# Kernel optimization log

Hardware: AMD Instinct MI355X
Metric: run time of the kernel (lower is better)

## Reference

```python
import jax, jax.numpy as jnp
import numpy as np
from jax import lax

H = 1024        # lstm_hidden_size
V = 512         # action_vocab_size
WV = 300        # word_vec_size
S = 64          # step_num
N = 512         # entity_num


def setup_inputs() -> dict:
    key = jax.random.key(0)
    ks = jax.random.split(key, 16)
    s = 0.02
    return {
        "video_vectors": jax.random.normal(ks[0], (1, S, H), jnp.float32),
        "entity_vectors": jax.random.normal(ks[1], (N, H), jnp.float32),
        # action_selector: Linear(H,H) -> ReLU -> Dropout(eval: identity) -> Linear(H,V) -> Sigmoid
        "A1w": jax.random.normal(ks[2], (H, H), jnp.float32) * s,
        "A1b": jnp.zeros((H,), jnp.float32),
        "A2w": jax.random.normal(ks[3], (V, H), jnp.float32) * s,
        "A2b": jnp.zeros((V,), jnp.float32),
        "action_emb": jax.random.normal(ks[4], (V, WV), jnp.float32) * s,
        "W1w": jax.random.normal(ks[5], (H, H), jnp.float32) * s,
        "W1b": jnp.zeros((H,), jnp.float32),
        "W2w": jax.random.normal(ks[6], (H, H + V), jnp.float32) * s,
        "W2b": jnp.zeros((H,), jnp.float32),
        "W3w": jax.random.normal(ks[7], (3, H), jnp.float32) * s,
        "W3b": jnp.zeros((3,), jnp.float32),
        "W4w": jax.random.normal(ks[8], (1, WV), jnp.float32) * s,
        "W4b": jnp.zeros((1,), jnp.float32),
    }


def _forward(video_vectors, entity_vectors, A1w, A1b, A2w, A2b, action_emb,
             W1w, W1b, W2w, W2b, W3w, W3b, W4w, W4b):
    vv = video_vectors[0]                       # [S, H]
    n = entity_vectors.shape[0]

    def step(carry, v_ac):
        ev, prev_ent_attn = carry               # ev: [N, H], prev: [N]
        # action selector (dropout is identity in eval)
        h = jax.nn.relu(v_ac @ A1w.T + A1b)
        ac_prob = jax.nn.sigmoid(h @ A2w.T + A2b)        # [V]
        bar_ft = (ac_prob / ac_prob.sum()) @ action_emb  # [WV]
        hat_ht = jax.nn.relu(v_ac @ W1w.T + W1b)         # [H]
        w2v = jnp.concatenate([hat_ht, ac_prob]) @ W2w.T + W2b  # [H]
        ent_prob = jax.nn.sigmoid(ev @ w2v)              # [N]
        choice = jax.nn.softmax(hat_ht @ W3w.T + W3b)    # [3]
        attn = choice[0] * ent_prob + choice[1] * prev_ent_attn  # (choice[2]*0)
        bar_et = (attn / attn.sum()) @ ev                # [H]
        scal = bar_ft @ W4w[0] + W4b[0]                  # scalar (W4(bar_ft))
        kt = jax.nn.relu(scal * bar_et)                  # [H]
        ev_new = attn[:, None] * kt[None, :] + (1.0 - attn)[:, None] * ev  # [N, H]
        return (ev_new, ent_prob), (ent_prob, ac_prob, bar_et, ev_new, bar_ft)

    init = (entity_vectors, jnp.zeros((n,), entity_vectors.dtype))
    _, (ent_probs, ac_probs, step_ent, step_all, step_act) = lax.scan(step, init, vv)
    return ent_probs, ac_probs, step_ent, step_all, step_act


def reference(video_vectors, entity_vectors, A1w, A1b, A2w, A2b, action_emb,
              W1w, W1b, W2w, W2b, W3w, W3b, W4w, W4b):
    return _forward(video_vectors, entity_vectors, A1w, A1b, A2w, A2b, action_emb,
                    W1w, W1b, W2w, W2b, W3w, W3b, W4w, W4b)
```

## Files before the change

### kernel.cpp

```cpp
#include <hip/hip_runtime.h>

#define H  1024
#define V  512
#define WV 300
#define S  64
#define N  512

#define WS_HALL   0
#define WS_CAT    (S*H)
#define WS_W2V    (WS_CAT + S*1536)
#define WS_CHOICE (WS_W2V + S*H)
#define WS_SCAL   (WS_CHOICE + 2*S)
#define WS_ACSUM  (WS_SCAL + S)
#define WS_KT     (WS_ACSUM + S)
#define WS_ATT    (WS_KT + S*H)
#define WS_ACCUM  (WS_ATT + S*N)
#define WS_ASUM   (WS_ACCUM + 3*H)
#define WS_CTR    (WS_ASUM + 4)

#define OUT_EP   0
#define OUT_AC   (S*N)
#define OUT_SE   (S*N + S*V)
#define OUT_ALL  (OUT_SE + S*H)
#define OUT_ACT  (OUT_ALL + (size_t)S*N*H)

__device__ __forceinline__ float wave_reduce(float v) {
#pragma unroll
  for (int m = 32; m > 0; m >>= 1) v += __shfl_xor(v, m, 64);
  return v;
}
__device__ __forceinline__ float dot4(float4 a, float4 b) {
  return a.x*b.x + a.y*b.y + a.z*b.z + a.w*b.w;
}

#define KC 64
__global__ __launch_bounds__(256) void gemmNT(
    const float* __restrict__ X, int ldx,
    const float* __restrict__ W, const float* __restrict__ bias,
    int K, int act,
    float* __restrict__ out1, int ld1,
    float* __restrict__ out2, int ld2) {
  __shared__ float Xs[64][KC + 4];
  __shared__ float Ws[64][KC + 4];
  const int tid = threadIdx.x;
  const int tm = tid >> 5, tn = tid & 31;
  const int jbase = blockIdx.x * 64;
  float acc[8][2];
#pragma unroll
  for (int i = 0; i < 8; ++i) acc[i][0] = acc[i][1] = 0.f;
  const int lr = tid >> 2;
  const int lc = (tid & 3) * 16;
  for (int k0 = 0; k0 < K; k0 += KC) {
    const float4* xp = (const float4*)(X + (size_t)lr * ldx + k0 + lc);
    const float4* wp = (const float4*)(W + (size_t)(jbase + lr) * K + k0 + lc);
    float4 xv0 = xp[0], xv1 = xp[1], xv2 = xp[2], xv3 = xp[3];
    float4 wv0 = wp[0], wv1 = wp[1], wv2 = wp[2], wv3 = wp[3];
    __syncthreads();
    *(float4*)&Xs[lr][lc +  0] = xv0; *(float4*)&Xs[lr][lc +  4] = xv1;
    *(float4*)&Xs[lr][lc +  8] = xv2; *(float4*)&Xs[lr][lc + 12] = xv3;
    *(float4*)&Ws[lr][lc +  0] = wv0; *(float4*)&Ws[lr][lc +  4] = wv1;
    *(float4*)&Ws[lr][lc +  8] = wv2; *(float4*)&Ws[lr][lc + 12] = wv3;
    __syncthreads();
#pragma unroll
    for (int kk = 0; kk < KC; kk += 4) {
      float4 w0 = *(const float4*)&Ws[tn][kk];
      float4 w1 = *(const float4*)&Ws[tn + 32][kk];
#pragma unroll
      for (int i = 0; i < 8; ++i) {
        float4 x = *(const float4*)&Xs[tm * 8 + i][kk];
        acc[i][0] += dot4(x, w0);
        acc[i][1] += dot4(x, w1);
      }
    }
  }
  const int j0 = jbase + tn, j1 = jbase + tn + 32;
  const float b0 = bias[j0], b1 = bias[j1];
#pragma unroll
  for (int i = 0; i < 8; ++i) {
    const int r = tm * 8 + i;
    float v0 = acc[i][0] + b0;
    float v1 = acc[i][1] + b1;
    if (act == 1) { v0 = fmaxf(v0, 0.f); v1 = fmaxf(v1, 0.f); }
    else if (act == 2) {
      v0 = 1.f / (1.f + __expf(-v0));
      v1 = 1.f / (1.f + __expf(-v1));
    }
    out1[(size_t)r * ld1 + j0] = v0;
    out1[(size_t)r * ld1 + j1] = v1;
    if (out2) {
      out2[(size_t)r * ld2 + j0] = v0;
      out2[(size_t)r * ld2 + j1] = v1;
    }
  }
}

__global__ void k_choice(const float* __restrict__ cat, const float* __restrict__ out_ac,
                         const float* __restrict__ W3w, const float* __restrict__ W3b,
                         float* __restrict__ ws) {
  int t = blockIdx.x, tid = threadIdx.x;
  const float* hat = cat + (size_t)t * 1536;
  float4 h4 = *(const float4*)(hat + tid * 4);
  float p[4];
#pragma unroll
  for (int r = 0; r < 3; ++r) {
    float4 w4 = *(const float4*)(W3w + (size_t)r * H + tid * 4);
    p[r] = dot4(h4, w4);
  }
  const float* ac = out_ac + (size_t)t * V;
  p[3] = ac[tid * 2] + ac[tid * 2 + 1];
  __shared__ float red[4][256];
#pragma unroll
  for (int q = 0; q < 4; ++q) red[q][tid] = p[q];
  __syncthreads();
  for (int sft = 128; sft > 0; sft >>= 1) {
    if (tid < sft) {
#pragma unroll
      for (int q = 0; q < 4; ++q) red[q][tid] += red[q][tid + sft];
    }
    __syncthreads();
  }
  if (tid == 0) {
    float l0 = red[0][0] + W3b[0], l1 = red[1][0] + W3b[1], l2 = red[2][0] + W3b[2];
    float m  = fmaxf(l0, fmaxf(l1, l2));
    float e0 = __expf(l0 - m), e1 = __expf(l1 - m), e2 = __expf(l2 - m);
    float inv = 1.f / (e0 + e1 + e2);
    ws[WS_CHOICE + t * 2]     = e0 * inv;
    ws[WS_CHOICE + t * 2 + 1] = e1 * inv;
    ws[WS_ACSUM + t]          = red[3][0];
  }
}

__global__ __launch_bounds__(256) void k_barft(
    const float* __restrict__ out_ac, const float* __restrict__ emb,
    const float* __restrict__ ws_ro, const float* __restrict__ W4w,
    const float* __restrict__ W4b, float* __restrict__ out_act,
    float* __restrict__ ws) {
  int t = blockIdx.x, tid = threadIdx.x;
  __shared__ float acS[V];
  const float* ac = out_ac + (size_t)t * V;
  acS[tid] = ac[tid];
  acS[tid + 256] = ac[tid + 256];
  __syncthreads();
  float s0 = 0.f, s1 = 0.f;
  const int w0 = tid, w1 = 256 + tid;
  for (int v = 0; v < V; ++v) {
    float a = acS[v];
    const float* er = emb + (size_t)v * WV;
    s0 += a * er[w0];
    if (tid < WV - 256) s1 += a * er[w1];
  }
  float inv = 1.f / ws_ro[WS_ACSUM + t];
  s0 *= inv; s1 *= inv;
  out_act[(size_t)t * WV + w0] = s0;
  if (tid < WV - 256) out_act[(size_t)t * WV + w1] = s1;
  float p = s0 * W4w[w0] + (tid < WV - 256 ? s1 * W4w[w1] : 0.f);
  __shared__ float red[256];
  red[tid] = p;
  __syncthreads();
  for (int s = 128; s > 0; s >>= 1) {
    if (tid < s) red[tid] += red[tid + s];
    __syncthreads();
  }
  if (tid == 0) ws[WS_SCAL + t] = red[0] + W4b[0];
}

__global__ __launch_bounds__(256) void k_seq(
    const float* __restrict__ ev0, const float* __restrict__ ws,
    float* __restrict__ accum, float* __restrict__ asum, unsigned* __restrict__ ctr,
    float* __restrict__ att, float* __restrict__ ktb,
    float* __restrict__ out_ep, float* __restrict__ out_se) {
  const int g = blockIdx.x, tid = threadIdx.x;
  const int lane = tid & 63, wv = tid >> 6;
  const int col = tid * 4;
  __shared__ float attnS[8], prevS[8], red[8][4];
  if (tid < 8) prevS[tid] = 0.f;
  float4 ev[8];
#pragma unroll
  for (int r = 0; r < 8; ++r)
    ev[r] = *(const float4*)(ev0 + (size_t)(g * 8 + r) * H + col);
  __syncthreads();
  unsigned target = 0;
  for (int t = 0; t < S; ++t) {
    const float4 w4 = *(const float4*)(ws + WS_W2V + (size_t)t * H + col);
    float dp[8];
#pragma unroll
    for (int r = 0; r < 8; ++r) dp[r] = dot4(ev[r], w4);
#pragma unroll
    for (int r = 0; r < 8; ++r) {
#pragma unroll
      for (int m = 32; m > 0; m >>= 1) dp[r] += __shfl_xor(dp[r], m, 64);
    }
    if (lane == 0) {
#pragma unroll
      for (int r = 0; r < 8; ++r) red[r][wv] = dp[r];
    }
    __syncthreads();
    if (tid < 8) {
      float d  = red[tid][0] + red[tid][1] + red[tid][2] + red[tid][3];
      float ep = 1.f / (1.f + __expf(-d));
      out_ep[(size_t)t * N + g * 8 + tid] = ep;
      float a = ws[WS_CHOICE + 2 * t] * ep + ws[WS_CHOICE + 2 * t + 1] * prevS[tid];
      prevS[tid] = ep;
      attnS[tid] = a;
      att[(size_t)t * N + g * 8 + tid] = a;
    }
    __syncthreads();
    float at[8];
#pragma unroll
    for (int r = 0; r < 8; ++r) at[r] = attnS[r];
    float4 pv = make_float4(0.f, 0.f, 0.f, 0.f);
#pragma unroll
    for (int r = 0; r < 8; ++r) {
      pv.x += at[r] * ev[r].x; pv.y += at[r] * ev[r].y;
      pv.z += at[r] * ev[r].z; pv.w += at[r] * ev[r].w;
    }
    float* acc = accum + (t % 3) * H;
    atomicAdd(acc + col + 0, pv.x);
    atomicAdd(acc + col + 1, pv.y);
    atomicAdd(acc + col + 2, pv.z);
    atomicAdd(acc + col + 3, pv.w);
    if (tid == 0) {
      float pa = 0.f;
#pragma unroll
      for (int r = 0; r < 8; ++r) pa += at[r];
      atomicAdd(asum + (t % 3), pa);
    }
    __syncthreads();
    target += (unsigned)gridDim.x;
    if (tid == 0) {
      __hip_atomic_fetch_add(ctr, 1u, __ATOMIC_RELEASE, __HIP_MEMORY_SCOPE_AGENT);
      while (__hip_atomic_load(ctr, __ATOMIC_ACQUIRE, __HIP_MEMORY_SCOPE_AGENT) < target)
        __builtin_amdgcn_s_sleep(2);
    }
    __syncthreads();
    float asv = __hip_atomic_load(asum + (t % 3), __ATOMIC_RELAXED, __HIP_MEMORY_SCOPE_AGENT);
    float4 pvs;
    pvs.x = __hip_atomic_load(acc + col + 0, __ATOMIC_RELAXED, __HIP_MEMORY_SCOPE_AGENT);
    pvs.y = __hip_atomic_load(acc + col + 1, __ATOMIC_RELAXED, __HIP_MEMORY_SCOPE_AGENT);
    pvs.z = __hip_atomic_load(acc + col + 2, __ATOMIC_RELAXED, __HIP_MEMORY_SCOPE_AGENT);
    pvs.w = __hip_atomic_load(acc + col + 3, __ATOMIC_RELAXED, __HIP_MEMORY_SCOPE_AGENT);
    float inv = 1.f / asv;
    float4 bar = make_float4(pvs.x * inv, pvs.y * inv, pvs.z * inv, pvs.w * inv);
    float sc = ws[WS_SCAL + t];
    float4 kt = make_float4(fmaxf(sc * bar.x, 0.f), fmaxf(sc * bar.y, 0.f),
                            fmaxf(sc * bar.z, 0.f), fmaxf(sc * bar.w, 0.f));
    if (g == 0) {
      *(float4*)(out_se + (size_t)t * H + col) = bar;
      *(float4*)(ktb + (size_t)t * H + col) = kt;
    }
    if (tid < 16)
      __hip_atomic_store(accum + ((t + 2) % 3) * H + g * 16 + tid, 0.f,
                         __ATOMIC_RELAXED, __HIP_MEMORY_SCOPE_AGENT);
    if (g == 0 && tid == 16)
      __hip_atomic_store(asum + ((t + 2) % 3), 0.f, __ATOMIC_RELAXED, __HIP_MEMORY_SCOPE_AGENT);
#pragma unroll
    for (int r = 0; r < 8; ++r) {
      float a = at[r];
      ev[r].x = a * kt.x + (1.f - a) * ev[r].x;
      ev[r].y = a * kt.y + (1.f - a) * ev[r].y;
      ev[r].z = a * kt.z + (1.f - a) * ev[r].z;
      ev[r].w = a * kt.w + (1.f - a) * ev[r].w;
    }
  }
}

__global__ __launch_bounds__(256) void k_recon(
    const float* __restrict__ ev0, const float* __restrict__ att,
    const float* __restrict__ ktb, float* __restrict__ out_all) {
  const int n = blockIdx.x, tid = threadIdx.x;
  const int col = tid * 4;
  __shared__ float aS[S];
  if (tid < S) aS[tid] = att[(size_t)tid * N + n];
  float4 v = *(const float4*)(ev0 + (size_t)n * H + col);
  __syncthreads();
  for (int t = 0; t < S; ++t) {
    float a = aS[t];
    float4 k4 = *(const float4*)(ktb + (size_t)t * H + col);
    v.x = a * k4.x + (1.f - a) * v.x;
    v.y = a * k4.y + (1.f - a) * v.y;
    v.z = a * k4.z + (1.f - a) * v.z;
    v.w = a * k4.w + (1.f - a) * v.w;
    *(float4*)(out_all + ((size_t)t * N + n) * H + col) = v;
  }
}

extern "C" void kernel_launch(void* const* d_in, const int* in_sizes, int n_in,
                              void* d_out, int out_size, void* d_ws, size_t ws_size,
                              hipStream_t stream) {
  const float* vv  = (const float*)d_in[0];
  const float* ev0 = (const float*)d_in[1];
  const float* A1w = (const float*)d_in[2];
  const float* A1b = (const float*)d_in[3];
  const float* A2w = (const float*)d_in[4];
  const float* A2b = (const float*)d_in[5];
  const float* emb = (const float*)d_in[6];
  const float* W1w = (const float*)d_in[7];
  const float* W1b = (const float*)d_in[8];
  const float* W2w = (const float*)d_in[9];
  const float* W2b = (const float*)d_in[10];
  const float* W3w = (const float*)d_in[11];
  const float* W3b = (const float*)d_in[12];
  const float* W4w = (const float*)d_in[13];
  const float* W4b = (const float*)d_in[14];

  float* ws  = (float*)d_ws;
  float* out = (float*)d_out;
  float* out_ep  = out + OUT_EP;
  float* out_ac  = out + OUT_AC;
  float* out_se  = out + OUT_SE;
  float* out_all = out + OUT_ALL;
  float* out_act = out + OUT_ACT;
  float* cat = ws + WS_CAT;

  hipMemsetAsync(ws + WS_ACCUM, 0, (size_t)(3 * H + 5) * sizeof(float), stream);

  gemmNT<<<16, 256, 0, stream>>>(vv, H, A1w, A1b, H, 1, ws + WS_HALL, H, (float*)nullptr, 0);
  gemmNT<<<16, 256, 0, stream>>>(vv, H, W1w, W1b, H, 1, cat, 1536, (float*)nullptr, 0);
  gemmNT<<<8, 256, 0, stream>>>(ws + WS_HALL, H, A2w, A2b, H, 2, out_ac, V, cat + H, 1536);
  k_choice<<<S, 256, 0, stream>>>(cat, out_ac, W3w, W3b, ws);
  gemmNT<<<16, 256, 0, stream>>>(cat, 1536, W2w, W2b, 1536, 0, ws + WS_W2V, H, (float*)nullptr, 0);
  k_barft<<<S, 256, 0, stream>>>(out_ac, emb, ws, W4w, W4b, out_act, ws);
  k_seq<<<64, 256, 0, stream>>>(ev0, ws, ws + WS_ACCUM, ws + WS_ASUM,
                                (unsigned*)(ws + WS_CTR),
                                ws + WS_ATT, ws + WS_KT, out_ep, out_se);
  k_recon<<<N, 256, 0, stream>>>(ev0, ws + WS_ATT, ws + WS_KT, out_all);
}
```

Measured before the change: 1.380 ms.

## Batch input GEMMs into one launch, prefetch K tiles, spin without sleep

Merges the two independent GEMMs on the video vectors (A1 and W1) into a single launch using a 2D grid, which removes one kernel launch and lets both run concurrently. It also adds register prefetch of the next K chunk in the GEMM so global loads overlap with the shared-memory compute. The grid barrier in the sequential kernel now busy-spins with relaxed loads and no s_sleep, then does one acquire load, which should shorten barrier wake-up latency across 64 steps at the cost of heavier polling traffic.

After: 1.267 ms. 1.09x faster.

```diff
diff --git a/kernel.cpp b/kernel.cpp
--- a/kernel.cpp
+++ b/kernel.cpp
@@ -24,25 +24,31 @@
 #define OUT_ALL  (OUT_SE + S*H)
 #define OUT_ACT  (OUT_ALL + (size_t)S*N*H)
 
-__device__ __forceinline__ float wave_reduce(float v) {
-#pragma unroll
-  for (int m = 32; m > 0; m >>= 1) v += __shfl_xor(v, m, 64);
-  return v;
-}
 __device__ __forceinline__ float dot4(float4 a, float4 b) {
   return a.x*b.x + a.y*b.y + a.z*b.z + a.w*b.w;
 }
 
+struct GArgs {
+  const float* X; const float* W0; const float* W1;
+  const float* B0; const float* B1;
+  float* o1_0; float* o1_1; float* o2_0; float* o2_1;
+  int ldx, K, act, ld1_0, ld1_1, ld2_0, ld2_1;
+};
+
 #define KC 64
-__global__ __launch_bounds__(256) void gemmNT(
-    const float* __restrict__ X, int ldx,
-    const float* __restrict__ W, const float* __restrict__ bias,
-    int K, int act,
-    float* __restrict__ out1, int ld1,
-    float* __restrict__ out2, int ld2) {
+__global__ __launch_bounds__(256) void gemmNT(GArgs a) {
   __shared__ float Xs[64][KC + 4];
   __shared__ float Ws[64][KC + 4];
   const int tid = threadIdx.x;
+  const int m = blockIdx.y;
+  const float* W    = m ? a.W1 : a.W0;
+  const float* bias = m ? a.B1 : a.B0;
+  float* out1 = m ? a.o1_1 : a.o1_0;
+  float* out2 = m ? a.o2_1 : a.o2_0;
+  const int ld1 = m ? a.ld1_1 : a.ld1_0;
+  const int ld2 = m ? a.ld2_1 : a.ld2_0;
+  const int K = a.K;
+
   const int tm = tid >> 5, tn = tid & 31;
   const int jbase = blockIdx.x * 64;
   float acc[8][2];
@@ -50,17 +56,28 @@
   for (int i = 0; i < 8; ++i) acc[i][0] = acc[i][1] = 0.f;
   const int lr = tid >> 2;
   const int lc = (tid & 3) * 16;
+  const float* xrow = a.X + (size_t)lr * a.ldx + lc;
+  const float* wrow = W + (size_t)(jbase + lr) * K + lc;
+  float4 xv0, xv1, xv2, xv3, wv0, wv1, wv2, wv3;
+  xv0 = ((const float4*)xrow)[0]; xv1 = ((const float4*)xrow)[1];
+  xv2 = ((const float4*)xrow)[2]; xv3 = ((const float4*)xrow)[3];
+  wv0 = ((const float4*)wrow)[0]; wv1 = ((const float4*)wrow)[1];
+  wv2 = ((const float4*)wrow)[2]; wv3 = ((const float4*)wrow)[3];
   for (int k0 = 0; k0 < K; k0 += KC) {
-    const float4* xp = (const float4*)(X + (size_t)lr * ldx + k0 + lc);
-    const float4* wp = (const float4*)(W + (size_t)(jbase + lr) * K + k0 + lc);
-    float4 xv0 = xp[0], xv1 = xp[1], xv2 = xp[2], xv3 = xp[3];
-    float4 wv0 = wp[0], wv1 = wp[1], wv2 = wp[2], wv3 = wp[3];
     __syncthreads();
     *(float4*)&Xs[lr][lc +  0] = xv0; *(float4*)&Xs[lr][lc +  4] = xv1;
     *(float4*)&Xs[lr][lc +  8] = xv2; *(float4*)&Xs[lr][lc + 12] = xv3;
     *(float4*)&Ws[lr][lc +  0] = wv0; *(float4*)&Ws[lr][lc +  4] = wv1;
     *(float4*)&Ws[lr][lc +  8] = wv2; *(float4*)&Ws[lr][lc + 12] = wv3;
     __syncthreads();
+    if (k0 + KC < K) {
+      const float* xp = xrow + k0 + KC;
+      const float* wp = wrow + k0 + KC;
+      xv0 = ((const float4*)xp)[0]; xv1 = ((const float4*)xp)[1];
+      xv2 = ((const float4*)xp)[2]; xv3 = ((const float4*)xp)[3];
+      wv0 = ((const float4*)wp)[0]; wv1 = ((const float4*)wp)[1];
+      wv2 = ((const float4*)wp)[2]; wv3 = ((const float4*)wp)[3];
+    }
 #pragma unroll
     for (int kk = 0; kk < KC; kk += 4) {
       float4 w0 = *(const float4*)&Ws[tn][kk];
@@ -80,8 +97,8 @@
     const int r = tm * 8 + i;
     float v0 = acc[i][0] + b0;
     float v1 = acc[i][1] + b1;
-    if (act == 1) { v0 = fmaxf(v0, 0.f); v1 = fmaxf(v1, 0.f); }
-    else if (act == 2) {
+    if (a.act == 1) { v0 = fmaxf(v0, 0.f); v1 = fmaxf(v1, 0.f); }
+    else if (a.act == 2) {
       v0 = 1.f / (1.f + __expf(-v0));
       v1 = 1.f / (1.f + __expf(-v1));
     }
@@ -229,8 +246,8 @@
     target += (unsigned)gridDim.x;
     if (tid == 0) {
       __hip_atomic_fetch_add(ctr, 1u, __ATOMIC_RELEASE, __HIP_MEMORY_SCOPE_AGENT);
-      while (__hip_atomic_load(ctr, __ATOMIC_ACQUIRE, __HIP_MEMORY_SCOPE_AGENT) < target)
-        __builtin_amdgcn_s_sleep(2);
+      while (__hip_atomic_load(ctr, __ATOMIC_RELAXED, __HIP_MEMORY_SCOPE_AGENT) < target) {}
+      (void)__hip_atomic_load(ctr, __ATOMIC_ACQUIRE, __HIP_MEMORY_SCOPE_AGENT);
     }
     __syncthreads();
     float asv = __hip_atomic_load(asum + (t % 3), __ATOMIC_RELAXED, __HIP_MEMORY_SCOPE_AGENT);
@@ -314,11 +331,28 @@
 
   hipMemsetAsync(ws + WS_ACCUM, 0, (size_t)(3 * H + 5) * sizeof(float), stream);
 
-  gemmNT<<<16, 256, 0, stream>>>(vv, H, A1w, A1b, H, 1, ws + WS_HALL, H, (float*)nullptr, 0);
-  gemmNT<<<16, 256, 0, stream>>>(vv, H, W1w, W1b, H, 1, cat, 1536, (float*)nullptr, 0);
-  gemmNT<<<8, 256, 0, stream>>>(ws + WS_HALL, H, A2w, A2b, H, 2, out_ac, V, cat + H, 1536);
+  {
+    GArgs a{};
+    a.X = vv; a.ldx = H; a.K = H; a.act = 1;
+    a.W0 = A1w; a.B0 = A1b; a.o1_0 = ws + WS_HALL; a.ld1_0 = H;   a.o2_0 = nullptr; a.ld2_0 = 0;
+    a.W1 = W1w; a.B1 = W1b; a.o1_1 = cat;          a.ld1_1 = 1536; a.o2_1 = nullptr; a.ld2_1 = 0;
+    gemmNT<<<dim3(16, 2), 256, 0, stream>>>(a);
+  }
+  {
+    GArgs a{};
+    a.X = ws + WS_HALL; a.ldx = H; a.K = H; a.act = 2;
+    a.W0 = A2w; a.B0 = A2b; a.o1_0 = out_ac; a.ld1_0 = V; a.o2_0 = cat + H; a.ld2_0 = 1536;
+    a.W1 = A2w; a.B1 = A2b; a.o1_1 = out_ac; a.ld1_1 = V; a.o2_1 = cat + H; a.ld2_1 = 1536;
+    gemmNT<<<dim3(8, 1), 256, 0, stream>>>(a);
+  }
   k_choice<<<S, 256, 0, stream>>>(cat, out_ac, W3w, W3b, ws);
-  gemmNT<<<16, 256, 0, stream>>>(cat, 1536, W2w, W2b, 1536, 0, ws + WS_W2V, H, (float*)nullptr, 0);
+  {
+    GArgs a{};
+    a.X = cat; a.ldx = 1536; a.K = 1536; a.act = 0;
+    a.W0 = W2w; a.B0 = W2b; a.o1_0 = ws + WS_W2V; a.ld1_0 = H; a.o2_0 = nullptr; a.ld2_0 = 0;
+    a.W1 = W2w; a.B1 = W2b; a.o1_1 = ws + WS_W2V; a.ld1_1 = H; a.o2_1 = nullptr; a.ld2_1 = 0;
+    gemmNT<<<dim3(16, 1), 256, 0, stream>>>(a);
+  }
   k_barft<<<S, 256, 0, stream>>>(out_ac, emb, ws, W4w, W4b, out_act, ws);
   k_seq<<<64, 256, 0, stream>>>(ev0, ws, ws + WS_ACCUM, ws + WS_ASUM,
                                 (unsigned*)(ws + WS_CTR),
```
